# Performance work log

Measured on AMD Instinct MI355X. Metric: run time of the kernel, lower is better.

Reference implementation:

```python
import jax, jax.numpy as jnp
import numpy as np

H = 16  # num_heads

def setup_inputs() -> dict:
    key = jax.random.key(0)
    ks = jax.random.split(key, 9)
    B, S, E = 2, 2048, 1024
    d = E // H  # 64, shared KV head dim
    sc = lambda n: 1.0 / np.sqrt(n)
    return {
        "x": jax.random.normal(ks[0], (B, S, E), jnp.float32),
        "wq": jax.random.normal(ks[1], (E, E), jnp.float32) * sc(E),
        "bq": jax.random.normal(ks[2], (E,), jnp.float32) * 0.02,
        "wk": jax.random.normal(ks[3], (E, d), jnp.float32) * sc(E),
        "bk": jax.random.normal(ks[4], (d,), jnp.float32) * 0.02,
        "wv": jax.random.normal(ks[5], (E, d), jnp.float32) * sc(E),
        "bv": jax.random.normal(ks[6], (d,), jnp.float32) * 0.02,
        "wo": jax.random.normal(ks[7], (E, E), jnp.float32) * sc(E),
        "bo": jax.random.normal(ks[8], (E,), jnp.float32) * 0.02,
    }

def reference(x, wq, bq, wk, bk, wv, bv, wo, bo):
    B, S, E = x.shape
    d = E // H
    Q = (x @ wq + bq).reshape(B, S, H, d).transpose(0, 2, 1, 3)  # [B,H,S,d]
    K = x @ wk + bk  # [B,S,d] shared across heads (MQA)
    V = x @ wv + bv  # [B,S,d]
    scores = jnp.einsum('bhqd,bkd->bhqk', Q, K) / np.sqrt(d)  # [B,H,S,S]
    weights = jax.nn.softmax(scores, axis=-1)
    attn = jnp.einsum('bhqk,bkd->bhqd', weights, V)  # [B,H,S,d]
    # FAITHFUL to source: reshape [B,H,S,d] -> [B,S,E] WITHOUT permuting back
    attn = attn.reshape(B, S, E)
    return attn @ wo + bo
```

## Files before the change

kernel.cpp:

```cpp
#include <hip/hip_runtime.h>
#include <hip/hip_bf16.h>

#define BB 2
#define SS 2048
#define EE 1024
#define HH 16
#define DD 64

using bfrag  = __attribute__((ext_vector_type(8))) short;
using bfrag4 = __attribute__((ext_vector_type(4))) short;
using ffrag  = __attribute__((ext_vector_type(4))) float;
using uint2v = __attribute__((ext_vector_type(2))) uint;

#define MFMA32(A, B, C) __builtin_amdgcn_mfma_f32_16x16x32_bf16(A, B, C, 0, 0, 0)
#define MFMA16(A, B, C) __builtin_amdgcn_mfma_f32_16x16x16bf16_1k(A, B, C, 0, 0, 0)

static __device__ __forceinline__ ushort f2bf(float f) {
  __hip_bfloat16 h = __float2bfloat16(f);
  return *reinterpret_cast<ushort*>(&h);
}

static __device__ __forceinline__ uint pack_bf2(float lo, float hi) {
  uint a = __float_as_uint(lo) + 0x8000u;
  uint b = __float_as_uint(hi) + 0x8000u;
  return __builtin_amdgcn_perm(b, a, 0x07060302u);
}

static __device__ __forceinline__ void gl_lds16(const ushort* g, ushort* l) {
  __builtin_amdgcn_global_load_lds(
      (const __attribute__((address_space(1))) void*)g,
      (__attribute__((address_space(3))) void*)l, 16, 0, 0);
}

__global__ __launch_bounds__(256) void prep(
    const float* __restrict__ x, const float* __restrict__ wq,
    const float* __restrict__ wk, const float* __restrict__ wv,
    const float* __restrict__ wo, ushort* __restrict__ xb,
    ushort* __restrict__ wqkvT, ushort* __restrict__ woT) {
  __shared__ float t[32][33];
  int id = blockIdx.x;
  if (id < 4096) {
    int i = id * 256 + threadIdx.x;
    float4 v = ((const float4*)x)[i];
    ushort4 u = { f2bf(v.x), f2bf(v.y), f2bf(v.z), f2bf(v.w) };
    ((ushort4*)xb)[i] = u;
    return;
  }
  id -= 4096;
  const float* src;
  ushort* dst;
  int N, bx, by;
  if (id < 1024)      { src = wq; dst = wqkvT;                      N = 1024; bx = id & 31;          by = id >> 5; }
  else if (id < 2048) { src = wo; dst = woT;                        N = 1024; bx = (id - 1024) & 31; by = (id - 1024) >> 5; }
  else if (id < 2112) { src = wk; dst = wqkvT + (size_t)1024 * 1024; N = 64;  bx = (id - 2048) & 1;  by = (id - 2048) >> 1; }
  else                { src = wv; dst = wqkvT + (size_t)1088 * 1024; N = 64;  bx = (id - 2112) & 1;  by = (id - 2112) >> 1; }
  const int k0 = by * 32, n0 = bx * 32;
  const int tx = threadIdx.x & 31, ty = threadIdx.x >> 5;
  #pragma unroll
  for (int i = 0; i < 32; i += 8)
    t[ty + i][tx] = src[(size_t)(k0 + ty + i) * N + n0 + tx];
  __syncthreads();
  #pragma unroll
  for (int i = 0; i < 32; i += 8)
    dst[(size_t)(n0 + ty + i) * 1024 + k0 + tx] = f2bf(t[tx][ty + i]);
}

template <bool QKV>
__global__ __launch_bounds__(256) void gemm_mfma3(
    const ushort* __restrict__ A, const ushort* __restrict__ Bt,
    const float* __restrict__ bias0, const float* __restrict__ bias1,
    const float* __restrict__ bias2, void* __restrict__ O1,
    ushort* __restrict__ Kb, ushort* __restrict__ VTb,
    int M, int N, int K, float qscale) {
  __shared__ __align__(16) ushort As[2][128 * 64];
  __shared__ __align__(16) ushort Bs[2][64 * 64];
  const int tid = threadIdx.x;
  const int lane = tid & 63;
  const int quad = lane >> 4;
  const int c = lane & 15;
  const int wv = tid >> 6;
  const int wm = (wv & 1) * 64;
  const int wn = (wv >> 1) * 32;
  const size_t m0 = (size_t)blockIdx.y * 128;
  const size_t n0 = (size_t)blockIdx.x * 64;

  const int srow = lane >> 3;
  const int sck = (lane & 7) ^ srow;

  ffrag zero = {0.f, 0.f, 0.f, 0.f};
  ffrag acc[4][2];
  #pragma unroll
  for (int mt = 0; mt < 4; ++mt)
    #pragma unroll
    for (int nt = 0; nt < 2; ++nt) acc[mt][nt] = zero;

  const int NK = K >> 6;
  #pragma unroll
  for (int i = 0; i < 4; ++i) {
    int ia = wv * 4 + i;
    gl_lds16(&A[(m0 + ia * 8 + srow) * (size_t)K + sck * 8], &As[0][ia * 512]);
  }
  #pragma unroll
  for (int i = 0; i < 2; ++i) {
    int ib = wv * 2 + i;
    gl_lds16(&Bt[(n0 + ib * 8 + srow) * (size_t)K + sck * 8], &Bs[0][ib * 512]);
  }
  __syncthreads();

  for (int ki = 0; ki < NK; ++ki) {
    const int buf = ki & 1;
    if (ki + 1 < NK) {
      int k0 = (ki + 1) << 6;
      #pragma unroll
      for (int i = 0; i < 4; ++i) {
        int ia = wv * 4 + i;
        gl_lds16(&A[(m0 + ia * 8 + srow) * (size_t)K + k0 + sck * 8],
                 &As[buf ^ 1][ia * 512]);
      }
      #pragma unroll
      for (int i = 0; i < 2; ++i) {
        int ib = wv * 2 + i;
        gl_lds16(&Bt[(n0 + ib * 8 + srow) * (size_t)K + k0 + sck * 8],
                 &Bs[buf ^ 1][ib * 512]);
      }
    }
    #pragma unroll
    for (int ks = 0; ks < 2; ++ks) {
      bfrag af[4], bf[2];
      #pragma unroll
      for (int mt = 0; mt < 4; ++mt) {
        int ra = wm + mt * 16 + c;
        af[mt] = *(const bfrag*)&As[buf][(ra * 8 + ((ks * 4 + quad) ^ (ra & 7))) * 8];
      }
      #pragma unroll
      for (int nt = 0; nt < 2; ++nt) {
        int rb = wn + nt * 16 + c;
        bf[nt] = *(const bfrag*)&Bs[buf][(rb * 8 + ((ks * 4 + quad) ^ (rb & 7))) * 8];
      }
      #pragma unroll
      for (int mt = 0; mt < 4; ++mt)
        #pragma unroll
        for (int nt = 0; nt < 2; ++nt)
          acc[mt][nt] = MFMA32(af[mt], bf[nt], acc[mt][nt]);
    }
    __syncthreads();
  }

  #pragma unroll
  for (int nt = 0; nt < 2; ++nt) {
    const int colb = (int)n0 + wn + nt * 16;
    if (QKV) {
      if (colb < 1024) {
        float bb = bias0[colb + c];
        ushort* dst = (ushort*)O1 + colb;
        #pragma unroll
        for (int mt = 0; mt < 4; ++mt)
          #pragma unroll
          for (int r = 0; r < 4; ++r) {
            size_t row = m0 + wm + mt * 16 + quad * 4 + r;
            dst[row * 1024 + c] = f2bf((acc[mt][nt][r] + bb) * qscale);
          }
      } else if (colb < 1088) {
        float bb = bias1[colb - 1024 + c];
        ushort* dst = Kb + (colb - 1024);
        #pragma unroll
        for (int mt = 0; mt < 4; ++mt)
          #pragma unroll
          for (int r = 0; r < 4; ++r) {
            size_t row = m0 + wm + mt * 16 + quad * 4 + r;
            dst[row * 64 + c] = f2bf(acc[mt][nt][r] + bb);
          }
      } else {
        int d = colb - 1088 + c;
        float bb = bias2[colb - 1088 + c];
        int bidx = (int)(m0 >> 11);
        ushort* dstv = VTb + ((size_t)(bidx * 64 + d)) * SS;
        #pragma unroll
        for (int mt = 0; mt < 4; ++mt) {
          int sb = (int)(m0 & 2047) + wm + mt * 16 + quad * 4;
          uint2v u;
          u.x = pack_bf2(acc[mt][nt][0] + bb, acc[mt][nt][1] + bb);
          u.y = pack_bf2(acc[mt][nt][2] + bb, acc[mt][nt][3] + bb);
          *(uint2v*)&dstv[sb] = u;
        }
      }
    } else {
      float bb = bias0[colb + c];
      float* dst = (float*)O1;
      #pragma unroll
      for (int mt = 0; mt < 4; ++mt)
        #pragma unroll
        for (int r = 0; r < 4; ++r) {
          size_t row = m0 + wm + mt * 16 + quad * 4 + r;
          dst[row * (size_t)N + colb + c] = acc[mt][nt][r] + bb;
        }
    }
  }
}

__global__ __launch_bounds__(256) void mqa_attn8(
    const ushort* __restrict__ Q, const ushort* __restrict__ Kg,
    const ushort* __restrict__ VT, ushort* __restrict__ A2) {
  __shared__ __align__(16) ushort Kt[2][4096];
  __shared__ __align__(16) ushort Vt[2][4096];
  const int tid = threadIdx.x;
  const int lane = tid & 63;
  const int quad = lane >> 4;
  const int c = lane & 15;
  const int wv = tid >> 6;
  const int bid = blockIdx.x;
  const int b = bid >> 8;
  const int r = bid & 255;
  const int h = r >> 4;
  const int s0 = (r & 15) << 7;

  const int srow = lane >> 3;
  const int sck = (lane & 7) ^ srow;

  ffrag zero = {0.f, 0.f, 0.f, 0.f};
  bfrag4 ones4;
  #pragma unroll
  for (int i = 0; i < 4; ++i) ones4[i] = (short)16256;

  bfrag aq[2][2];
  #pragma unroll
  for (int mt = 0; mt < 2; ++mt) {
    const ushort* qp =
        Q + ((size_t)(b * SS) + s0 + wv * 32 + mt * 16 + c) * EE + h * 64 + quad * 8;
    aq[mt][0] = *(const bfrag*)qp;
    aq[mt][1] = *(const bfrag*)(qp + 32);
  }

  ffrag o[2][4];
  #pragma unroll
  for (int mt = 0; mt < 2; ++mt)
    #pragma unroll
    for (int nt = 0; nt < 4; ++nt) o[mt][nt] = zero;
  ffrag ls[2] = {zero, zero};

  const ushort* Kbase = Kg + (size_t)b * SS * 64;
  const ushort* Vbase = VT + (size_t)b * 64 * SS;
  const int i0 = wv * 2, i1 = wv * 2 + 1;
  const int r0 = i0 * 8 + srow, r1 = i1 * 8 + srow;

  gl_lds16(Kbase + (size_t)r0 * 64 + sck * 8, &Kt[0][i0 * 512]);
  gl_lds16(Kbase + (size_t)r1 * 64 + sck * 8, &Kt[0][i1 * 512]);
  gl_lds16(Vbase + (size_t)r0 * SS + sck * 8, &Vt[0][i0 * 512]);
  gl_lds16(Vbase + (size_t)r1 * SS + sck * 8, &Vt[0][i1 * 512]);
  __syncthreads();

  for (int it = 0; it < 32; ++it) {
    const int buf = it & 1;
    if (it + 1 < 32) {
      int kb = (it + 1) << 6;
      gl_lds16(Kbase + (size_t)(kb + r0) * 64 + sck * 8, &Kt[buf ^ 1][i0 * 512]);
      gl_lds16(Kbase + (size_t)(kb + r1) * 64 + sck * 8, &Kt[buf ^ 1][i1 * 512]);
      gl_lds16(Vbase + (size_t)r0 * SS + kb + sck * 8, &Vt[buf ^ 1][i0 * 512]);
      gl_lds16(Vbase + (size_t)r1 * SS + kb + sck * 8, &Vt[buf ^ 1][i1 * 512]);
    }

    #pragma unroll
    for (int kt = 0; kt < 4; ++kt) {
      const int key = kt * 16 + c;
      const int k7 = key & 7;
      bfrag kf0 = *(const bfrag*)&Kt[buf][(key * 8 + (quad ^ k7)) * 8];
      bfrag kf1 = *(const bfrag*)&Kt[buf][(key * 8 + ((quad + 4) ^ k7)) * 8];
      bfrag4 pb[2];
      #pragma unroll
      for (int mt = 0; mt < 2; ++mt) {
        ffrag st = MFMA32(kf0, aq[mt][0], zero);
        st = MFMA32(kf1, aq[mt][1], st);
        uint2v uu;
        uu.x = pack_bf2(__builtin_amdgcn_exp2f(st[0]),
                        __builtin_amdgcn_exp2f(st[1]));
        uu.y = pack_bf2(__builtin_amdgcn_exp2f(st[2]),
                        __builtin_amdgcn_exp2f(st[3]));
        pb[mt] = __builtin_bit_cast(bfrag4, uu);
      }
      const int ck = kt * 2 + (quad >> 1);
      const int wc = (quad & 1) * 4;
      #pragma unroll
      for (int nt = 0; nt < 4; ++nt) {
        int d = nt * 16 + c;
        bfrag4 vf = *(const bfrag4*)&Vt[buf][(d * 8 + (ck ^ (d & 7))) * 8 + wc];
        #pragma unroll
        for (int mt = 0; mt < 2; ++mt)
          o[mt][nt] = MFMA16(vf, pb[mt], o[mt][nt]);
      }
      #pragma unroll
      for (int mt = 0; mt < 2; ++mt)
        ls[mt] = MFMA16(ones4, pb[mt], ls[mt]);
    }
    __syncthreads();
  }

  #pragma unroll
  for (int mt = 0; mt < 2; ++mt) {
    const float inv = 1.f / ls[mt][0];
    const int sp = h * 128 + (s0 >> 4) + wv * 2 + mt;
    ushort* orow = A2 + ((size_t)b * SS + sp) * EE;
    #pragma unroll
    for (int nt = 0; nt < 4; ++nt) {
      uint2v u;
      u.x = pack_bf2(o[mt][nt][0] * inv, o[mt][nt][1] * inv);
      u.y = pack_bf2(o[mt][nt][2] * inv, o[mt][nt][3] * inv);
      *(uint2v*)&orow[c * 64 + nt * 16 + quad * 4] = u;
    }
  }
}

extern "C" void kernel_launch(void* const* d_in, const int* in_sizes, int n_in,
                              void* d_out, int out_size, void* d_ws, size_t ws_size,
                              hipStream_t stream) {
  const float* x  = (const float*)d_in[0];
  const float* wq = (const float*)d_in[1];
  const float* bq = (const float*)d_in[2];
  const float* wk = (const float*)d_in[3];
  const float* bk = (const float*)d_in[4];
  const float* wv = (const float*)d_in[5];
  const float* bv = (const float*)d_in[6];
  const float* wo = (const float*)d_in[7];
  const float* bo = (const float*)d_in[8];
  float* out = (float*)d_out;

  char* w = (char*)d_ws;
  ushort* xb     = (ushort*)w;  w += (size_t)4096 * 1024 * 2;
  ushort* wqkvT  = (ushort*)w;  w += (size_t)1152 * 1024 * 2;
  ushort* woT    = (ushort*)w;  w += (size_t)1024 * 1024 * 2;
  ushort* Qb     = (ushort*)w;  w += (size_t)4096 * 1024 * 2;
  ushort* Kb     = (ushort*)w;  w += (size_t)4096 * 64 * 2;
  ushort* VTb    = (ushort*)w;  w += (size_t)BB * 64 * SS * 2;
  ushort* A2     = (ushort*)w;  w += (size_t)4096 * 1024 * 2;

  prep<<<6272, 256, 0, stream>>>(x, wq, wk, wv, wo, xb, wqkvT, woT);

  const float qscale = 0.18033688011112042f;
  gemm_mfma3<true><<<dim3(18, 32), 256, 0, stream>>>(
      xb, wqkvT, bq, bk, bv, Qb, Kb, VTb, 4096, 1152, 1024, qscale);

  mqa_attn8<<<512, 256, 0, stream>>>(Qb, Kb, VTb, A2);

  gemm_mfma3<false><<<dim3(16, 32), 256, 0, stream>>>(
      A2, woT, bo, nullptr, nullptr, out, nullptr, nullptr, 4096, 1024, 1024, 1.0f);
}
```

Measured before the change: 183.2 us.

## Switch GEMMs to 128x128 tiles with BK=32 and M-major block order

The GEMM kernel now uses 128x128 output tiles with a K step of 32 instead of 128x64 tiles with a K step of 64. Each wave computes a 64x64 sub-tile (4x4 MFMA fragments), and the LDS swizzle is changed to suit 32-wide rows. The grid is transposed so consecutive blocks walk along M while sharing the same weight columns, which is meant to improve operand reuse and L2 locality. In exchange, the grid drops to 288 and 256 blocks (fewer than the CU count), each block needs more accumulator registers, and there are twice as many K iterations with barriers.

New measurement: 195.7 us. +6.8%, slower.

```diff
diff --git a/kernel.cpp b/kernel.cpp
--- a/kernel.cpp
+++ b/kernel.cpp
@@ -66,88 +66,70 @@
 }
 
 template <bool QKV>
-__global__ __launch_bounds__(256) void gemm_mfma3(
+__global__ __launch_bounds__(256) void gemm_mfma4(
     const ushort* __restrict__ A, const ushort* __restrict__ Bt,
     const float* __restrict__ bias0, const float* __restrict__ bias1,
     const float* __restrict__ bias2, void* __restrict__ O1,
     ushort* __restrict__ Kb, ushort* __restrict__ VTb,
     int M, int N, int K, float qscale) {
-  __shared__ __align__(16) ushort As[2][128 * 64];
-  __shared__ __align__(16) ushort Bs[2][64 * 64];
+  __shared__ __align__(16) ushort As[2][128 * 32];
+  __shared__ __align__(16) ushort Bs[2][128 * 32];
   const int tid = threadIdx.x;
   const int lane = tid & 63;
   const int quad = lane >> 4;
   const int c = lane & 15;
   const int wv = tid >> 6;
   const int wm = (wv & 1) * 64;
-  const int wn = (wv >> 1) * 32;
-  const size_t m0 = (size_t)blockIdx.y * 128;
-  const size_t n0 = (size_t)blockIdx.x * 64;
-
-  const int srow = lane >> 3;
-  const int sck = (lane & 7) ^ srow;
+  const int wn = (wv >> 1) * 64;
+  const size_t m0 = (size_t)blockIdx.x * 128;
+  const size_t n0 = (size_t)blockIdx.y * 128;
+
+  const int srow = lane >> 2;
+  const int skc = (lane & 3) ^ ((lane >> 3) & 3);
+  const int ia0 = wv * 2, ia1 = wv * 2 + 1;
+  const int ra0 = ia0 * 16 + srow, ra1 = ia1 * 16 + srow;
 
   ffrag zero = {0.f, 0.f, 0.f, 0.f};
-  ffrag acc[4][2];
+  ffrag acc[4][4];
   #pragma unroll
   for (int mt = 0; mt < 4; ++mt)
     #pragma unroll
-    for (int nt = 0; nt < 2; ++nt) acc[mt][nt] = zero;
-
-  const int NK = K >> 6;
-  #pragma unroll
-  for (int i = 0; i < 4; ++i) {
-    int ia = wv * 4 + i;
-    gl_lds16(&A[(m0 + ia * 8 + srow) * (size_t)K + sck * 8], &As[0][ia * 512]);
-  }
-  #pragma unroll
-  for (int i = 0; i < 2; ++i) {
-    int ib = wv * 2 + i;
-    gl_lds16(&Bt[(n0 + ib * 8 + srow) * (size_t)K + sck * 8], &Bs[0][ib * 512]);
-  }
+    for (int nt = 0; nt < 4; ++nt) acc[mt][nt] = zero;
+
+  const int NK = K >> 5;
+  gl_lds16(&A[(m0 + ra0) * (size_t)K + skc * 8], &As[0][ia0 * 512]);
+  gl_lds16(&A[(m0 + ra1) * (size_t)K + skc * 8], &As[0][ia1 * 512]);
+  gl_lds16(&Bt[(n0 + ra0) * (size_t)K + skc * 8], &Bs[0][ia0 * 512]);
+  gl_lds16(&Bt[(n0 + ra1) * (size_t)K + skc * 8], &Bs[0][ia1 * 512]);
   __syncthreads();
 
   for (int ki = 0; ki < NK; ++ki) {
     const int buf = ki & 1;
     if (ki + 1 < NK) {
-      int k0 = (ki + 1) << 6;
-      #pragma unroll
-      for (int i = 0; i < 4; ++i) {
-        int ia = wv * 4 + i;
-        gl_lds16(&A[(m0 + ia * 8 + srow) * (size_t)K + k0 + sck * 8],
-                 &As[buf ^ 1][ia * 512]);
-      }
-      #pragma unroll
-      for (int i = 0; i < 2; ++i) {
-        int ib = wv * 2 + i;
-        gl_lds16(&Bt[(n0 + ib * 8 + srow) * (size_t)K + k0 + sck * 8],
-                 &Bs[buf ^ 1][ib * 512]);
-      }
-    }
-    #pragma unroll
-    for (int ks = 0; ks < 2; ++ks) {
-      bfrag af[4], bf[2];
-      #pragma unroll
-      for (int mt = 0; mt < 4; ++mt) {
-        int ra = wm + mt * 16 + c;
-        af[mt] = *(const bfrag*)&As[buf][(ra * 8 + ((ks * 4 + quad) ^ (ra & 7))) * 8];
-      }
-      #pragma unroll
-      for (int nt = 0; nt < 2; ++nt) {
-        int rb = wn + nt * 16 + c;
-        bf[nt] = *(const bfrag*)&Bs[buf][(rb * 8 + ((ks * 4 + quad) ^ (rb & 7))) * 8];
-      }
-      #pragma unroll
-      for (int mt = 0; mt < 4; ++mt)
-        #pragma unroll
-        for (int nt = 0; nt < 2; ++nt)
-          acc[mt][nt] = MFMA32(af[mt], bf[nt], acc[mt][nt]);
-    }
+      int k0 = (ki + 1) << 5;
+      gl_lds16(&A[(m0 + ra0) * (size_t)K + k0 + skc * 8], &As[buf ^ 1][ia0 * 512]);
+      gl_lds16(&A[(m0 + ra1) * (size_t)K + k0 + skc * 8], &As[buf ^ 1][ia1 * 512]);
+      gl_lds16(&Bt[(n0 + ra0) * (size_t)K + k0 + skc * 8], &Bs[buf ^ 1][ia0 * 512]);
+      gl_lds16(&Bt[(n0 + ra1) * (size_t)K + k0 + skc * 8], &Bs[buf ^ 1][ia1 * 512]);
+    }
+    bfrag af[4], bf[4];
+    #pragma unroll
+    for (int t = 0; t < 4; ++t) {
+      int ra = wm + t * 16 + c;
+      af[t] = *(const bfrag*)&As[buf][(ra * 4 + (quad ^ ((ra >> 1) & 3))) * 8];
+      int rb = wn + t * 16 + c;
+      bf[t] = *(const bfrag*)&Bs[buf][(rb * 4 + (quad ^ ((rb >> 1) & 3))) * 8];
+    }
+    #pragma unroll
+    for (int mt = 0; mt < 4; ++mt)
+      #pragma unroll
+      for (int nt = 0; nt < 4; ++nt)
+        acc[mt][nt] = MFMA32(af[mt], bf[nt], acc[mt][nt]);
     __syncthreads();
   }
 
   #pragma unroll
-  for (int nt = 0; nt < 2; ++nt) {
+  for (int nt = 0; nt < 4; ++nt) {
     const int colb = (int)n0 + wn + nt * 16;
     if (QKV) {
       if (colb < 1024) {
@@ -335,11 +317,11 @@
   prep<<<6272, 256, 0, stream>>>(x, wq, wk, wv, wo, xb, wqkvT, woT);
 
   const float qscale = 0.18033688011112042f;
-  gemm_mfma3<true><<<dim3(18, 32), 256, 0, stream>>>(
+  gemm_mfma4<true><<<dim3(32, 9), 256, 0, stream>>>(
       xb, wqkvT, bq, bk, bv, Qb, Kb, VTb, 4096, 1152, 1024, qscale);
 
   mqa_attn8<<<512, 256, 0, stream>>>(Qb, Kb, VTb, A2);
 
-  gemm_mfma3<false><<<dim3(16, 32), 256, 0, stream>>>(
+  gemm_mfma4<false><<<dim3(32, 8), 256, 0, stream>>>(
       A2, woT, bo, nullptr, nullptr, out, nullptr, nullptr, 4096, 1024, 1024, 1.0f);
 }
```
